# Kernel optimization log

Measured on AMD Instinct MI355X. Metric: run time of the kernel, lower is better.

## Reference

```python
import jax, jax.numpy as jnp
import numpy as np
from jax import lax

EPS = 1e-12
CLS_K = 100   # cls-token prefilter size (hardcoded in patch_reconstruction)
ALPHA = 0.6   # weighting of cls vs patch-EMD distance (hardcoded in source)


def _l2norm(x, axis):
    # torch.nn.functional.normalize: x / max(||x||_2, eps)
    n = jnp.sqrt(jnp.sum(x * x, axis=axis, keepdims=True))
    return x / jnp.maximum(n, EPS)


def setup_inputs() -> dict:
    key = jax.random.key(0)
    k1, k2, k3, k4 = jax.random.split(key, 4)
    B, N, C, G = 16, 128, 768, 2000
    return {
        "query_cls": jax.random.normal(k1, (B, C), dtype=jnp.float32),
        "query_patch": jax.random.normal(k2, (B, N, C), dtype=jnp.float32),
        "gallery_memory_cls": jax.random.normal(k3, (G, 1, C), dtype=jnp.float32),
        "gallery_memory_patch": jax.random.normal(k4, (G, N, C), dtype=jnp.float32),
        "top_k": 10,
    }


def reference(query_cls, query_patch, gallery_memory_cls, gallery_memory_patch, top_k):
    B, N, C = query_patch.shape
    g_cls = gallery_memory_cls[:, 0, :]          # [G, C] (torch.squeeze)
    g_cls_n = _l2norm(g_cls, axis=1)             # normalize(gallery_feat, dim=1)

    def per_sample(qc, qp):
        # --- stage 1: cls-token cosine prefilter (find_k_neighbors, metric='cls_token')
        qc_n = _l2norm(qc, axis=0)               # [C]
        dist_cls_all = g_cls_n @ qc_n            # [G] cosine sim
        _, cls_idx = lax.top_k(dist_cls_all, CLS_K)   # top-100 by cls sim

        # --- stage 2: combined cls + patch-EMD score over the 100 candidates
        sq = _l2norm(qp.T, axis=0)               # [C, N] per-patch unit norm
        gp = gallery_memory_patch[cls_idx]       # [K, N, C] gather
        gp_t = _l2norm(jnp.transpose(gp, (0, 2, 1)), axis=1)  # [K, C, N]
        # pairwise patch cosine sims: [K, Nq, Ng]
        sim = jnp.einsum('cn,kcm->knm', sq, gp_t)
        # bidirectional Chamfer similarity as the patch-EMD score
        dist_emd = 0.5 * (jnp.mean(jnp.max(sim, axis=2), axis=1)
                          + jnp.mean(jnp.max(sim, axis=1), axis=1))  # [K]
        dist_cls = dist_cls_all[cls_idx]         # [K]
        dist = ALPHA * dist_cls + (1.0 - ALPHA) * dist_emd
        _, emd_idx = lax.top_k(dist, top_k)      # top_k of 100 candidates
        nb = cls_idx[emd_idx]                    # [top_k] gallery indices

        # --- reconstruction: gather neighbor patches + mean neighbor cls
        patch = gallery_memory_patch[nb]         # [top_k, N, C]
        cls_m = jnp.mean(g_cls[nb], axis=0)      # [C]
        return patch.reshape(top_k * N, C), cls_m

    rec_patch, rec_cls = jax.vmap(per_sample)(query_cls, query_patch)
    return rec_patch, rec_cls[:, None, :]        # [B, top_k*N, C], [B, 1, C]
```

## Files before the change

kernel.cpp:

```cpp
#include <hip/hip_runtime.h>
#include <float.h>
#include <math.h>

#define B_ 16
#define N_ 128
#define C_ 768
#define G_ 2000
#define CK_ 100
#define ALPHA_ 0.6f
#define EPS_ 1e-12f

typedef __attribute__((ext_vector_type(8))) short bf16x8;
typedef __attribute__((ext_vector_type(16))) float f32x16;

__device__ inline float wave_sum_lane0(float s) {
  #pragma unroll
  for (int off = 32; off > 0; off >>= 1) s += __shfl_down(s, off);
  return s;
}
__device__ inline float wave_sum_all(float s) {
  #pragma unroll
  for (int off = 1; off < 64; off <<= 1) s += __shfl_xor(s, off);
  return s;
}

__device__ inline unsigned short bf16_rtn(float x) {
  unsigned u = __float_as_uint(x);
  u += 0x7fffu + ((u >> 16) & 1u);
  return (unsigned short)(u >> 16);
}
__device__ inline void split2(float x, unsigned short& h, unsigned short& l) {
  h = bf16_rtn(x);
  float r = x - __uint_as_float(((unsigned)h) << 16);
  l = bf16_rtn(r);
}
__device__ inline void csplit8(const float4& v0, const float4& v1,
                               uint4& h, uint4& l, float& sq) {
  float f[8] = {v0.x, v0.y, v0.z, v0.w, v1.x, v1.y, v1.z, v1.w};
  unsigned short hh[8], ll[8];
  #pragma unroll
  for (int i = 0; i < 8; ++i) {
    float x = f[i];
    sq = fmaf(x, x, sq);
    split2(x, hh[i], ll[i]);
  }
  h.x = (unsigned)hh[0] | ((unsigned)hh[1] << 16);
  h.y = (unsigned)hh[2] | ((unsigned)hh[3] << 16);
  h.z = (unsigned)hh[4] | ((unsigned)hh[5] << 16);
  h.w = (unsigned)hh[6] | ((unsigned)hh[7] << 16);
  l.x = (unsigned)ll[0] | ((unsigned)ll[1] << 16);
  l.y = (unsigned)ll[2] | ((unsigned)ll[3] << 16);
  l.z = (unsigned)ll[4] | ((unsigned)ll[5] << 16);
  l.w = (unsigned)ll[6] | ((unsigned)ll[7] << 16);
}

#define NCLSBLK_ (B_ * G_ / 4)
__global__ void prep_kernel(const float* __restrict__ gcls, const float* __restrict__ qcls,
                            const float* __restrict__ qp,
                            float* __restrict__ dall,
                            unsigned short* __restrict__ qhi, unsigned short* __restrict__ qlo) {
  int t = threadIdx.x;
  int lane = t & 63;
  if ((int)blockIdx.x < NCLSBLK_) {
    int id = ((int)blockIdx.x * 256 + t) >> 6;
    int b = id / G_, g = id - b * G_;
    const float4* gv = (const float4*)(gcls + (size_t)g * C_);
    const float4* qv = (const float4*)(qcls + (size_t)b * C_);
    float sgq = 0.f, sgg = 0.f, sqq = 0.f;
    #pragma unroll
    for (int i = 0; i < 3; ++i) {
      float4 x = gv[lane + 64 * i], y = qv[lane + 64 * i];
      sgq += x.x * y.x + x.y * y.y + x.z * y.z + x.w * y.w;
      sgg += x.x * x.x + x.y * x.y + x.z * x.z + x.w * x.w;
      sqq += y.x * y.x + y.y * y.y + y.z * y.z + y.w * y.w;
    }
    sgq = wave_sum_lane0(sgq);
    sgg = wave_sum_lane0(sgg);
    sqq = wave_sum_lane0(sqq);
    if (lane == 0) {
      float gi = 1.0f / fmaxf(sqrtf(sgg), EPS_);
      float qi = 1.0f / fmaxf(sqrtf(sqq), EPS_);
      dall[id] = sgq * gi * qi;
    }
  } else {
    int wid = (((int)blockIdx.x - NCLSBLK_) * 256 + t) >> 6;
    const float4* v = (const float4*)(qp + (size_t)wid * C_);
    float4 x0 = v[lane], x1 = v[lane + 64], x2 = v[lane + 128];
    float s = x0.x * x0.x + x0.y * x0.y + x0.z * x0.z + x0.w * x0.w
            + x1.x * x1.x + x1.y * x1.y + x1.z * x1.z + x1.w * x1.w
            + x2.x * x2.x + x2.y * x2.y + x2.z * x2.z + x2.w * x2.w;
    s = wave_sum_all(s);
    float inv = 1.0f / fmaxf(sqrtf(s), EPS_);
    float4 xs[3] = {x0, x1, x2};
    #pragma unroll
    for (int i = 0; i < 3; ++i) {
      float4 x = xs[i];
      x.x *= inv; x.y *= inv; x.z *= inv; x.w *= inv;
      ushort4 h, l;
      split2(x.x, h.x, l.x); split2(x.y, h.y, l.y);
      split2(x.z, h.z, l.z); split2(x.w, h.w, l.w);
      size_t off = (size_t)wid * C_ + (size_t)(lane + 64 * i) * 4;
      *(ushort4*)(qhi + off) = h;
      *(ushort4*)(qlo + off) = l;
    }
  }
}

__global__ void top100_kernel(const float* __restrict__ dall, int* __restrict__ cls_idx,
                              float* __restrict__ dsel) {
  __shared__ unsigned long long s[2048];
  int b = blockIdx.x, t = threadIdx.x;
  for (int i = t; i < 2048; i += 256) {
    unsigned long long y = 0xFFFFFFFFFFFFFFFFull;
    if (i < G_) {
      unsigned u = __float_as_uint(dall[b * G_ + i]);
      unsigned key = (u & 0x80000000u) ? ~u : (u | 0x80000000u);
      y = ~(((unsigned long long)key << 32) | (unsigned long long)(0xFFFFFFFFu - (unsigned)i));
    }
    s[i] = y;
  }
  __syncthreads();
  for (int k = 2; k <= 2048; k <<= 1) {
    for (int j = k >> 1; j > 0; j >>= 1) {
      for (int i = t; i < 2048; i += 256) {
        int l = i ^ j;
        if (l > i) {
          unsigned long long a = s[i], c = s[l];
          bool up = ((i & k) == 0);
          if ((a > c) == up) { s[i] = c; s[l] = a; }
        }
      }
      __syncthreads();
    }
  }
  for (int it = t; it < CK_; it += 256) {
    unsigned long long x = ~s[it];
    int idx = (int)(0xFFFFFFFFu - (unsigned)(x & 0xFFFFFFFFull));
    unsigned key = (unsigned)(x >> 32);
    unsigned u = (key & 0x80000000u) ? (key & 0x7FFFFFFFu) : ~key;
    cls_idx[b * CK_ + it] = idx;
    dsel[b * CK_ + it] = __uint_as_float(u);
  }
}

__global__ __launch_bounds__(256, 4) void emd_kernel(
    const unsigned short* __restrict__ qhi, const unsigned short* __restrict__ qlo,
    const float* __restrict__ gpat,
    const int* __restrict__ cls_idx, const float* __restrict__ dsel,
    float* __restrict__ dist) {
  __shared__ __align__(16) unsigned short sAhi[4096], sAlo[4096], sBhi[4096], sBlo[4096];
  float* red_row = (float*)&sAhi[0];
  float* red_col = (float*)&sAhi[512];
  float* bssp    = (float*)&sAhi[1024];
  float* binvp   = (float*)&sAhi[1536];

  int r = blockIdx.x;
  int xc = r & 7;
  int q = r >> 3;
  int b = 2 * xc + (q >= CK_ ? 1 : 0);
  int k = (q >= CK_) ? (q - CK_) : q;
  int blk = b * CK_ + k;
  int g = cls_idx[blk];

  const float* Bptr = gpat + (size_t)g * (N_ * C_);

  int t = threadIdx.x;
  int lane = t & 63, wv = t >> 6;
  int wr = wv >> 1, wc = wv & 1;
  int l31 = lane & 31, lhi = lane >> 5;

  int m_st = t >> 1, half = t & 1;
  const unsigned short* ahB = qhi + (size_t)(b * N_ + m_st) * C_ + half * 16;
  const unsigned short* alB = qlo + (size_t)(b * N_ + m_st) * C_ + half * 16;
  const float* bB = Bptr + (size_t)m_st * C_ + half * 16;
  int sw_st = (m_st >> 1) & 3;
  int e0 = m_st * 32 + (((2 * half + 0) ^ sw_st) << 3);
  int e1 = m_st * 32 + (((2 * half + 1) ^ sw_st) << 3);

  f32x16 acc00, acc01, acc10, acc11;
  #pragma unroll
  for (int e = 0; e < 16; ++e) { acc00[e] = 0.f; acc01[e] = 0.f; acc10[e] = 0.f; acc11[e] = 0.f; }

  int rA0 = 64 * wr + l31, rA1 = rA0 + 32;
  int rB0 = 64 * wc + l31, rB1 = rB0 + 32;
  int swF = (l31 >> 1) & 3;

  float4 cb0, cb1, cb2, cb3;
  cb0 = *(const float4*)(bB);      cb1 = *(const float4*)(bB + 4);
  cb2 = *(const float4*)(bB + 8);  cb3 = *(const float4*)(bB + 12);

  float bsq = 0.f;
  const int NT = C_ / 32;
  for (int kt = 0; kt < NT; ++kt) {
    __syncthreads();
    int o = kt * 32;
    uint4 va0 = *(const uint4*)(ahB + o);
    uint4 va1 = *(const uint4*)(ahB + o + 8);
    uint4 va2 = *(const uint4*)(alB + o);
    uint4 va3 = *(const uint4*)(alB + o + 8);
    uint4 h, l;
    csplit8(cb0, cb1, h, l, bsq);
    *(uint4*)&sBhi[e0] = h;  *(uint4*)&sBlo[e0] = l;
    csplit8(cb2, cb3, h, l, bsq);
    *(uint4*)&sBhi[e1] = h;  *(uint4*)&sBlo[e1] = l;
    *(uint4*)&sAhi[e0] = va0;  *(uint4*)&sAhi[e1] = va1;
    *(uint4*)&sAlo[e0] = va2;  *(uint4*)&sAlo[e1] = va3;
    if (kt + 1 < NT) {
      int o2 = o + 32;
      cb0 = *(const float4*)(bB + o2);       cb1 = *(const float4*)(bB + o2 + 4);
      cb2 = *(const float4*)(bB + o2 + 8);   cb3 = *(const float4*)(bB + o2 + 12);
    }
    __syncthreads();
    #pragma unroll
    for (int ks = 0; ks < 2; ++ks) {
      int so = (((ks * 2 + lhi) ^ swF) << 3);
      bf16x8 ah0 = *(const bf16x8*)&sAhi[rA0 * 32 + so];
      bf16x8 al0 = *(const bf16x8*)&sAlo[rA0 * 32 + so];
      bf16x8 ah1 = *(const bf16x8*)&sAhi[rA1 * 32 + so];
      bf16x8 al1 = *(const bf16x8*)&sAlo[rA1 * 32 + so];
      bf16x8 bh0 = *(const bf16x8*)&sBhi[rB0 * 32 + so];
      bf16x8 bl0 = *(const bf16x8*)&sBlo[rB0 * 32 + so];
      bf16x8 bh1 = *(const bf16x8*)&sBhi[rB1 * 32 + so];
      bf16x8 bl1 = *(const bf16x8*)&sBlo[rB1 * 32 + so];
      acc00 = __builtin_amdgcn_mfma_f32_32x32x16_bf16(ah0, bh0, acc00, 0, 0, 0);
      acc00 = __builtin_amdgcn_mfma_f32_32x32x16_bf16(ah0, bl0, acc00, 0, 0, 0);
      acc00 = __builtin_amdgcn_mfma_f32_32x32x16_bf16(al0, bh0, acc00, 0, 0, 0);
      acc01 = __builtin_amdgcn_mfma_f32_32x32x16_bf16(ah0, bh1, acc01, 0, 0, 0);
      acc01 = __builtin_amdgcn_mfma_f32_32x32x16_bf16(ah0, bl1, acc01, 0, 0, 0);
      acc01 = __builtin_amdgcn_mfma_f32_32x32x16_bf16(al0, bh1, acc01, 0, 0, 0);
      acc10 = __builtin_amdgcn_mfma_f32_32x32x16_bf16(ah1, bh0, acc10, 0, 0, 0);
      acc10 = __builtin_amdgcn_mfma_f32_32x32x16_bf16(ah1, bl0, acc10, 0, 0, 0);
      acc10 = __builtin_amdgcn_mfma_f32_32x32x16_bf16(al1, bh0, acc10, 0, 0, 0);
      acc11 = __builtin_amdgcn_mfma_f32_32x32x16_bf16(ah1, bh1, acc11, 0, 0, 0);
      acc11 = __builtin_amdgcn_mfma_f32_32x32x16_bf16(ah1, bl1, acc11, 0, 0, 0);
      acc11 = __builtin_amdgcn_mfma_f32_32x32x16_bf16(al1, bh1, acc11, 0, 0, 0);
    }
  }
  __syncthreads();

  bssp[t] = bsq;
  __syncthreads();
  if (t < 128) {
    float s = bssp[2 * t] + bssp[2 * t + 1];
    binvp[t] = 1.0f / fmaxf(sqrtf(s), EPS_);
  }
  __syncthreads();
  float bi0 = binvp[64 * wc + l31];
  float bi1 = binvp[64 * wc + 32 + l31];

  {
    float rm[16];
    #pragma unroll
    for (int e = 0; e < 16; ++e) rm[e] = fmaxf(acc00[e] * bi0, acc01[e] * bi1);
    #pragma unroll
    for (int msk = 1; msk <= 16; msk <<= 1)
      #pragma unroll
      for (int e = 0; e < 16; ++e) rm[e] = fmaxf(rm[e], __shfl_xor(rm[e], msk));
    if (l31 == 0) {
      #pragma unroll
      for (int e = 0; e < 16; ++e)
        red_row[(64 * wr + (e & 3) + 8 * (e >> 2) + 4 * lhi) * 2 + wc] = rm[e];
    }
  }
  {
    float rm[16];
    #pragma unroll
    for (int e = 0; e < 16; ++e) rm[e] = fmaxf(acc10[e] * bi0, acc11[e] * bi1);
    #pragma unroll
    for (int msk = 1; msk <= 16; msk <<= 1)
      #pragma unroll
      for (int e = 0; e < 16; ++e) rm[e] = fmaxf(rm[e], __shfl_xor(rm[e], msk));
    if (l31 == 0) {
      #pragma unroll
      for (int e = 0; e < 16; ++e)
        red_row[(64 * wr + 32 + (e & 3) + 8 * (e >> 2) + 4 * lhi) * 2 + wc] = rm[e];
    }
  }
  {
    float cm0 = -FLT_MAX, cm1 = -FLT_MAX;
    #pragma unroll
    for (int e = 0; e < 16; ++e) {
      cm0 = fmaxf(cm0, fmaxf(acc00[e], acc10[e]));
      cm1 = fmaxf(cm1, fmaxf(acc01[e], acc11[e]));
    }
    cm0 = fmaxf(cm0, __shfl_xor(cm0, 32)) * bi0;
    cm1 = fmaxf(cm1, __shfl_xor(cm1, 32)) * bi1;
    if (lane < 32) {
      red_col[(64 * wc + lane) * 2 + wr] = cm0;
      red_col[(64 * wc + 32 + lane) * 2 + wr] = cm1;
    }
  }
  __syncthreads();
  if (t < 128)
    bssp[t] = fmaxf(red_row[2 * t], red_row[2 * t + 1]) +
              fmaxf(red_col[2 * t], red_col[2 * t + 1]);
  __syncthreads();
  if (t < 64) {
    float v = bssp[t] + bssp[t + 64];
    #pragma unroll
    for (int off = 32; off > 0; off >>= 1) v += __shfl_down(v, off);
    if (t == 0) {
      float emd = 0.5f * v * (1.0f / 128.0f);
      dist[blk] = ALPHA_ * dsel[blk] + (1.0f - ALPHA_) * emd;
    }
  }
}

__global__ void sel10_kernel(const float* __restrict__ dist, const int* __restrict__ cls_idx,
                             const float* __restrict__ gcls, float* __restrict__ out_cls,
                             int* __restrict__ nb, int TK) {
  int b = blockIdx.x, t = threadIdx.x;
  __shared__ float v[128];
  __shared__ int snb[64];
  if (t < 128) v[t] = (t < CK_) ? dist[b * CK_ + t] : -FLT_MAX;
  __syncthreads();
  for (int j = 0; j < TK; ++j) {
    if (t < 64) {
      float v0 = v[t], v1 = v[t + 64];
      float bv; int bi;
      if (v0 >= v1) { bv = v0; bi = t; } else { bv = v1; bi = t + 64; }
      #pragma unroll
      for (int off = 1; off < 64; off <<= 1) {
        float ov = __shfl_xor(bv, off);
        int   oi = __shfl_xor(bi, off);
        if (ov > bv || (ov == bv && oi < bi)) { bv = ov; bi = oi; }
      }
      if (t == 0) {
        int gg = cls_idx[b * CK_ + bi];
        snb[j] = gg;
        nb[b * TK + j] = gg;
        v[bi] = -FLT_MAX;
      }
    }
    __syncthreads();
  }
  float invk = 1.0f / (float)TK;
  for (int c = t; c < C_; c += 256) {
    float s = 0.f;
    for (int j = 0; j < TK; ++j) s += gcls[(size_t)snb[j] * C_ + c];
    out_cls[(size_t)b * C_ + c] = s * invk;
  }
}

__global__ void gather_kernel(const float* __restrict__ gpat, const int* __restrict__ nb,
                              float* __restrict__ out, int TK) {
  int i = blockIdx.x * blockDim.x + threadIdx.x;
  int per_vec = N_ * C_ / 4;
  int per_b = TK * per_vec;
  int total = B_ * per_b;
  if (i >= total) return;
  int b = i / per_b;
  int r = i - b * per_b;
  int j = r / per_vec;
  int off = r - j * per_vec;
  int g = nb[b * TK + j];
  ((float4*)out)[i] = ((const float4*)gpat)[(size_t)g * per_vec + off];
}

extern "C" void kernel_launch(void* const* d_in, const int* in_sizes, int n_in,
                              void* d_out, int out_size, void* d_ws, size_t ws_size,
                              hipStream_t stream) {
  (void)in_sizes; (void)n_in; (void)ws_size;
  const float* qcls = (const float*)d_in[0];
  const float* qpat = (const float*)d_in[1];
  const float* gcls = (const float*)d_in[2];
  const float* gpat = (const float*)d_in[3];
  int TK = (out_size / B_ - C_) / (N_ * C_);

  unsigned short* qhi = (unsigned short*)d_ws;
  unsigned short* qlo = qhi + (size_t)B_ * N_ * C_;
  float* dall  = (float*)(qlo + (size_t)B_ * N_ * C_);
  float* dsel  = dall + B_ * G_;
  float* dist  = dsel + B_ * CK_;
  int* cls_idx = (int*)(dist + B_ * CK_);
  int* nb      = cls_idx + B_ * CK_;

  hipLaunchKernelGGL(prep_kernel, dim3(NCLSBLK_ + B_ * N_ / 4), dim3(256), 0, stream,
                     gcls, qcls, qpat, dall, qhi, qlo);
  hipLaunchKernelGGL(top100_kernel, dim3(B_), dim3(256), 0, stream, dall, cls_idx, dsel);
  hipLaunchKernelGGL(emd_kernel, dim3(B_ * CK_), dim3(256), 0, stream,
                     qhi, qlo, gpat, cls_idx, dsel, dist);
  float* out_cls = (float*)d_out + (size_t)B_ * TK * N_ * C_;
  hipLaunchKernelGGL(sel10_kernel, dim3(B_), dim3(256), 0, stream,
                     dist, cls_idx, gcls, out_cls, nb, TK);
  int total4 = B_ * TK * (N_ * C_ / 4);
  hipLaunchKernelGGL(gather_kernel, dim3((total4 + 255) / 256), dim3(256), 0, stream,
                     gpat, nb, (float*)d_out, TK);
}
```

Baseline: 320.5 us.

## Use 512-thread blocks in EMD kernel with 8 waves each computing 64x32 tiles

Moves the EMD similarity kernel from 4 waves per block, each holding a 64x64 output tile, to 8 waves per block, each holding a 64x32 tile. The staging loads are spread over twice as many threads, and the query tile loads are now prefetched one step ahead along with the gallery loads. The per-row norm reduction and the row and column max reductions are rewritten for the new wave grid. The aim is more waves in flight to hide memory latency and fewer accumulator registers per thread, at the cost of more LDS reads per MFMA and a 512-thread launch bound that may limit how many blocks fit per CU.

```diff
diff --git a/kernel.cpp b/kernel.cpp
--- a/kernel.cpp
+++ b/kernel.cpp
@@ -143,16 +143,16 @@
   }
 }
 
-__global__ __launch_bounds__(256, 4) void emd_kernel(
+__global__ __launch_bounds__(512, 4) void emd_kernel(
     const unsigned short* __restrict__ qhi, const unsigned short* __restrict__ qlo,
     const float* __restrict__ gpat,
     const int* __restrict__ cls_idx, const float* __restrict__ dsel,
     float* __restrict__ dist) {
   __shared__ __align__(16) unsigned short sAhi[4096], sAlo[4096], sBhi[4096], sBlo[4096];
   float* red_row = (float*)&sAhi[0];
-  float* red_col = (float*)&sAhi[512];
-  float* bssp    = (float*)&sAhi[1024];
-  float* binvp   = (float*)&sAhi[1536];
+  float* red_col = (float*)&sAhi[1024];
+  float* bssp    = (float*)&sAhi[1536];
+  float* binvp   = (float*)&sAhi[1792];
 
   int r = blockIdx.x;
   int xc = r & 7;
@@ -166,49 +166,47 @@
 
   int t = threadIdx.x;
   int lane = t & 63, wv = t >> 6;
-  int wr = wv >> 1, wc = wv & 1;
+  int wr = wv >> 2, wc = wv & 3;
   int l31 = lane & 31, lhi = lane >> 5;
 
-  int m_st = t >> 1, half = t & 1;
-  const unsigned short* ahB = qhi + (size_t)(b * N_ + m_st) * C_ + half * 16;
-  const unsigned short* alB = qlo + (size_t)(b * N_ + m_st) * C_ + half * 16;
-  const float* bB = Bptr + (size_t)m_st * C_ + half * 16;
+  int m_st = t >> 2, quar = t & 3;
+  const unsigned short* ahB = qhi + (size_t)(b * N_ + m_st) * C_ + quar * 8;
+  const unsigned short* alB = qlo + (size_t)(b * N_ + m_st) * C_ + quar * 8;
+  const float* bB = Bptr + (size_t)m_st * C_ + quar * 8;
   int sw_st = (m_st >> 1) & 3;
-  int e0 = m_st * 32 + (((2 * half + 0) ^ sw_st) << 3);
-  int e1 = m_st * 32 + (((2 * half + 1) ^ sw_st) << 3);
-
-  f32x16 acc00, acc01, acc10, acc11;
+  int e0 = m_st * 32 + ((quar ^ sw_st) << 3);
+
+  f32x16 acc0, acc1;
   #pragma unroll
-  for (int e = 0; e < 16; ++e) { acc00[e] = 0.f; acc01[e] = 0.f; acc10[e] = 0.f; acc11[e] = 0.f; }
+  for (int e = 0; e < 16; ++e) { acc0[e] = 0.f; acc1[e] = 0.f; }
 
   int rA0 = 64 * wr + l31, rA1 = rA0 + 32;
-  int rB0 = 64 * wc + l31, rB1 = rB0 + 32;
+  int rB0 = 32 * wc + l31;
   int swF = (l31 >> 1) & 3;
 
-  float4 cb0, cb1, cb2, cb3;
-  cb0 = *(const float4*)(bB);      cb1 = *(const float4*)(bB + 4);
-  cb2 = *(const float4*)(bB + 8);  cb3 = *(const float4*)(bB + 12);
+  uint4 cah, cal;
+  float4 cb0, cb1;
+  cah = *(const uint4*)(ahB);
+  cal = *(const uint4*)(alB);
+  cb0 = *(const float4*)(bB);
+  cb1 = *(const float4*)(bB + 4);
 
   float bsq = 0.f;
   const int NT = C_ / 32;
   for (int kt = 0; kt < NT; ++kt) {
     __syncthreads();
-    int o = kt * 32;
-    uint4 va0 = *(const uint4*)(ahB + o);
-    uint4 va1 = *(const uint4*)(ahB + o + 8);
-    uint4 va2 = *(const uint4*)(alB + o);
-    uint4 va3 = *(const uint4*)(alB + o + 8);
+    *(uint4*)&sAhi[e0] = cah;
+    *(uint4*)&sAlo[e0] = cal;
     uint4 h, l;
     csplit8(cb0, cb1, h, l, bsq);
-    *(uint4*)&sBhi[e0] = h;  *(uint4*)&sBlo[e0] = l;
-    csplit8(cb2, cb3, h, l, bsq);
-    *(uint4*)&sBhi[e1] = h;  *(uint4*)&sBlo[e1] = l;
-    *(uint4*)&sAhi[e0] = va0;  *(uint4*)&sAhi[e1] = va1;
-    *(uint4*)&sAlo[e0] = va2;  *(uint4*)&sAlo[e1] = va3;
+    *(uint4*)&sBhi[e0] = h;
+    *(uint4*)&sBlo[e0] = l;
     if (kt + 1 < NT) {
-      int o2 = o + 32;
-      cb0 = *(const float4*)(bB + o2);       cb1 = *(const float4*)(bB + o2 + 4);
-      cb2 = *(const float4*)(bB + o2 + 8);   cb3 = *(const float4*)(bB + o2 + 12);
+      int o = (kt + 1) * 32;
+      cah = *(const uint4*)(ahB + o);
+      cal = *(const uint4*)(alB + o);
+      cb0 = *(const float4*)(bB + o);
+      cb1 = *(const float4*)(bB + o + 4);
     }
     __syncthreads();
     #pragma unroll
@@ -220,38 +218,26 @@
       bf16x8 al1 = *(const bf16x8*)&sAlo[rA1 * 32 + so];
       bf16x8 bh0 = *(const bf16x8*)&sBhi[rB0 * 32 + so];
       bf16x8 bl0 = *(const bf16x8*)&sBlo[rB0 * 32 + so];
-      bf16x8 bh1 = *(const bf16x8*)&sBhi[rB1 * 32 + so];
-      bf16x8 bl1 = *(const bf16x8*)&sBlo[rB1 * 32 + so];
-      acc00 = __builtin_amdgcn_mfma_f32_32x32x16_bf16(ah0, bh0, acc00, 0, 0, 0);
-      acc00 = __builtin_amdgcn_mfma_f32_32x32x16_bf16(ah0, bl0, acc00, 0, 0, 0);
-      acc00 = __builtin_amdgcn_mfma_f32_32x32x16_bf16(al0, bh0, acc00, 0, 0, 0);
-      acc01 = __builtin_amdgcn_mfma_f32_32x32x16_bf16(ah0, bh1, acc01, 0, 0, 0);
-      acc01 = __builtin_amdgcn_mfma_f32_32x32x16_bf16(ah0, bl1, acc01, 0, 0, 0);
-      acc01 = __builtin_amdgcn_mfma_f32_32x32x16_bf16(al0, bh1, acc01, 0, 0, 0);
-      acc10 = __builtin_amdgcn_mfma_f32_32x32x16_bf16(ah1, bh0, acc10, 0, 0, 0);
-      acc10 = __builtin_amdgcn_mfma_f32_32x32x16_bf16(ah1, bl0, acc10, 0, 0, 0);
-      acc10 = __builtin_amdgcn_mfma_f32_32x32x16_bf16(al1, bh0, acc10, 0, 0, 0);
-      acc11 = __builtin_amdgcn_mfma_f32_32x32x16_bf16(ah1, bh1, acc11, 0, 0, 0);
-      acc11 = __builtin_amdgcn_mfma_f32_32x32x16_bf16(ah1, bl1, acc11, 0, 0, 0);
-      acc11 = __builtin_amdgcn_mfma_f32_32x32x16_bf16(al1, bh1, acc11, 0, 0, 0);
-    }
-  }
-  __syncthreads();
-
-  bssp[t] = bsq;
-  __syncthreads();
-  if (t < 128) {
-    float s = bssp[2 * t] + bssp[2 * t + 1];
-    binvp[t] = 1.0f / fmaxf(sqrtf(s), EPS_);
-  }
-  __syncthreads();
-  float bi0 = binvp[64 * wc + l31];
-  float bi1 = binvp[64 * wc + 32 + l31];
+      acc0 = __builtin_amdgcn_mfma_f32_32x32x16_bf16(ah0, bh0, acc0, 0, 0, 0);
+      acc0 = __builtin_amdgcn_mfma_f32_32x32x16_bf16(ah0, bl0, acc0, 0, 0, 0);
+      acc0 = __builtin_amdgcn_mfma_f32_32x32x16_bf16(al0, bh0, acc0, 0, 0, 0);
+      acc1 = __builtin_amdgcn_mfma_f32_32x32x16_bf16(ah1, bh0, acc1, 0, 0, 0);
+      acc1 = __builtin_amdgcn_mfma_f32_32x32x16_bf16(ah1, bl0, acc1, 0, 0, 0);
+      acc1 = __builtin_amdgcn_mfma_f32_32x32x16_bf16(al1, bh0, acc1, 0, 0, 0);
+    }
+  }
+  __syncthreads();
+
+  bsq += __shfl_xor(bsq, 1);
+  bsq += __shfl_xor(bsq, 2);
+  if ((t & 3) == 0) binvp[m_st] = 1.0f / fmaxf(sqrtf(bsq), EPS_);
+  __syncthreads();
+  float bi0 = binvp[rB0];
 
   {
     float rm[16];
     #pragma unroll
-    for (int e = 0; e < 16; ++e) rm[e] = fmaxf(acc00[e] * bi0, acc01[e] * bi1);
+    for (int e = 0; e < 16; ++e) rm[e] = acc0[e] * bi0;
     #pragma unroll
     for (int msk = 1; msk <= 16; msk <<= 1)
       #pragma unroll
@@ -259,13 +245,13 @@
     if (l31 == 0) {
       #pragma unroll
       for (int e = 0; e < 16; ++e)
-        red_row[(64 * wr + (e & 3) + 8 * (e >> 2) + 4 * lhi) * 2 + wc] = rm[e];
+        red_row[(64 * wr + (e & 3) + 8 * (e >> 2) + 4 * lhi) * 4 + wc] = rm[e];
     }
   }
   {
     float rm[16];
     #pragma unroll
-    for (int e = 0; e < 16; ++e) rm[e] = fmaxf(acc10[e] * bi0, acc11[e] * bi1);
+    for (int e = 0; e < 16; ++e) rm[e] = acc1[e] * bi0;
     #pragma unroll
     for (int msk = 1; msk <= 16; msk <<= 1)
       #pragma unroll
@@ -273,27 +259,23 @@
     if (l31 == 0) {
       #pragma unroll
       for (int e = 0; e < 16; ++e)
-        red_row[(64 * wr + 32 + (e & 3) + 8 * (e >> 2) + 4 * lhi) * 2 + wc] = rm[e];
+        red_row[(64 * wr + 32 + (e & 3) + 8 * (e >> 2) + 4 * lhi) * 4 + wc] = rm[e];
     }
   }
   {
-    float cm0 = -FLT_MAX, cm1 = -FLT_MAX;
-    #pragma unroll
-    for (int e = 0; e < 16; ++e) {
-      cm0 = fmaxf(cm0, fmaxf(acc00[e], acc10[e]));
-      cm1 = fmaxf(cm1, fmaxf(acc01[e], acc11[e]));
-    }
-    cm0 = fmaxf(cm0, __shfl_xor(cm0, 32)) * bi0;
-    cm1 = fmaxf(cm1, __shfl_xor(cm1, 32)) * bi1;
-    if (lane < 32) {
-      red_col[(64 * wc + lane) * 2 + wr] = cm0;
-      red_col[(64 * wc + 32 + lane) * 2 + wr] = cm1;
-    }
-  }
-  __syncthreads();
-  if (t < 128)
-    bssp[t] = fmaxf(red_row[2 * t], red_row[2 * t + 1]) +
-              fmaxf(red_col[2 * t], red_col[2 * t + 1]);
+    float cm = -FLT_MAX;
+    #pragma unroll
+    for (int e = 0; e < 16; ++e) cm = fmaxf(cm, fmaxf(acc0[e], acc1[e]));
+    cm = fmaxf(cm, __shfl_xor(cm, 32)) * bi0;
+    if (lane < 32) red_col[(32 * wc + lane) * 2 + wr] = cm;
+  }
+  __syncthreads();
+  if (t < 128) {
+    float r4 = fmaxf(fmaxf(red_row[4 * t], red_row[4 * t + 1]),
+                     fmaxf(red_row[4 * t + 2], red_row[4 * t + 3]));
+    float c2 = fmaxf(red_col[2 * t], red_col[2 * t + 1]);
+    bssp[t] = r4 + c2;
+  }
   __syncthreads();
   if (t < 64) {
     float v = bssp[t] + bssp[t + 64];
@@ -378,7 +360,7 @@
   hipLaunchKernelGGL(prep_kernel, dim3(NCLSBLK_ + B_ * N_ / 4), dim3(256), 0, stream,
                      gcls, qcls, qpat, dall, qhi, qlo);
   hipLaunchKernelGGL(top100_kernel, dim3(B_), dim3(256), 0, stream, dall, cls_idx, dsel);
-  hipLaunchKernelGGL(emd_kernel, dim3(B_ * CK_), dim3(256), 0, stream,
+  hipLaunchKernelGGL(emd_kernel, dim3(B_ * CK_), dim3(512), 0, stream,
                      qhi, qlo, gpat, cls_idx, dsel, dist);
   float* out_cls = (float*)d_out + (size_t)B_ * TK * N_ * C_;
   hipLaunchKernelGGL(sel10_kernel, dim3(B_), dim3(256), 0, stream,
```

Result: faster. 312.4 us (-2.5%).

## Double-buffer LDS tiles in EMD kernel and use truncation for bf16 split

Applied to the files above, without the earlier changes.

The EMD GEMM main loop now uses two LDS buffers, so staging the next K-tile overlaps with the MFMA work on the current one, with one barrier per tile instead of two. Global loads for B are prefetched two tiles ahead in alternating register sets. The hi/lo bf16 split now truncates the high part instead of rounding to nearest, which cuts integer ALU work but changes precision behaviour slightly (the lo residual is also truncated). LDS use doubles to 64KB and launch bounds drop to 2 blocks per CU, which may reduce occupancy.

```diff
diff --git a/kernel.cpp b/kernel.cpp
--- a/kernel.cpp
+++ b/kernel.cpp
@@ -34,24 +34,24 @@
   float r = x - __uint_as_float(((unsigned)h) << 16);
   l = bf16_rtn(r);
 }
-__device__ inline void csplit8(const float4& v0, const float4& v1,
+__device__ inline void tsplit8(const float4& v0, const float4& v1,
                                uint4& h, uint4& l, float& sq) {
   float f[8] = {v0.x, v0.y, v0.z, v0.w, v1.x, v1.y, v1.z, v1.w};
-  unsigned short hh[8], ll[8];
+  unsigned hu[4], lu[4];
   #pragma unroll
-  for (int i = 0; i < 8; ++i) {
-    float x = f[i];
-    sq = fmaf(x, x, sq);
-    split2(x, hh[i], ll[i]);
-  }
-  h.x = (unsigned)hh[0] | ((unsigned)hh[1] << 16);
-  h.y = (unsigned)hh[2] | ((unsigned)hh[3] << 16);
-  h.z = (unsigned)hh[4] | ((unsigned)hh[5] << 16);
-  h.w = (unsigned)hh[6] | ((unsigned)hh[7] << 16);
-  l.x = (unsigned)ll[0] | ((unsigned)ll[1] << 16);
-  l.y = (unsigned)ll[2] | ((unsigned)ll[3] << 16);
-  l.z = (unsigned)ll[4] | ((unsigned)ll[5] << 16);
-  l.w = (unsigned)ll[6] | ((unsigned)ll[7] << 16);
+  for (int p = 0; p < 4; ++p) {
+    float x0 = f[2 * p], x1 = f[2 * p + 1];
+    sq = fmaf(x0, x0, sq);
+    sq = fmaf(x1, x1, sq);
+    unsigned u0 = __float_as_uint(x0), u1 = __float_as_uint(x1);
+    float r0 = x0 - __uint_as_float(u0 & 0xFFFF0000u);
+    float r1 = x1 - __uint_as_float(u1 & 0xFFFF0000u);
+    unsigned v0b = __float_as_uint(r0), v1b = __float_as_uint(r1);
+    hu[p] = (u0 >> 16) | (u1 & 0xFFFF0000u);
+    lu[p] = (v0b >> 16) | (v1b & 0xFFFF0000u);
+  }
+  h = make_uint4(hu[0], hu[1], hu[2], hu[3]);
+  l = make_uint4(lu[0], lu[1], lu[2], lu[3]);
 }
 
 #define NCLSBLK_ (B_ * G_ / 4)
@@ -143,16 +143,17 @@
   }
 }
 
-__global__ __launch_bounds__(256, 4) void emd_kernel(
+__global__ __launch_bounds__(256, 2) void emd_kernel(
     const unsigned short* __restrict__ qhi, const unsigned short* __restrict__ qlo,
     const float* __restrict__ gpat,
     const int* __restrict__ cls_idx, const float* __restrict__ dsel,
     float* __restrict__ dist) {
-  __shared__ __align__(16) unsigned short sAhi[4096], sAlo[4096], sBhi[4096], sBlo[4096];
-  float* red_row = (float*)&sAhi[0];
-  float* red_col = (float*)&sAhi[512];
-  float* bssp    = (float*)&sAhi[1024];
-  float* binvp   = (float*)&sAhi[1536];
+  __shared__ __align__(16) unsigned short sAhi[2][4096], sAlo[2][4096];
+  __shared__ __align__(16) unsigned short sBhi[2][4096], sBlo[2][4096];
+  float* red_row = (float*)&sAhi[0][0];
+  float* red_col = (float*)&sAhi[0][512];
+  float* bssf    = (float*)&sAhi[0][1024];
+  float* binvf   = (float*)&sAhi[0][1536];
 
   int r = blockIdx.x;
   int xc = r & 7;
@@ -185,68 +186,96 @@
   int rB0 = 64 * wc + l31, rB1 = rB0 + 32;
   int swF = (l31 >> 1) & 3;
 
-  float4 cb0, cb1, cb2, cb3;
-  cb0 = *(const float4*)(bB);      cb1 = *(const float4*)(bB + 4);
-  cb2 = *(const float4*)(bB + 8);  cb3 = *(const float4*)(bB + 12);
+  const int NT = C_ / 32;
 
   float bsq = 0.f;
-  const int NT = C_ / 32;
-  for (int kt = 0; kt < NT; ++kt) {
+
+  uint4 cah0, cah1, cal0, cal1;
+  float4 bx0, bx1, bx2, bx3, by0, by1, by2, by3;
+
+#define LOAD_A(T) { int oA = (T) * 32;                                        \
+    cah0 = *(const uint4*)(ahB + oA);  cah1 = *(const uint4*)(ahB + oA + 8);  \
+    cal0 = *(const uint4*)(alB + oA);  cal1 = *(const uint4*)(alB + oA + 8); }
+#define LOAD_BX(T) { int oB = (T) * 32;                                       \
+    bx0 = *(const float4*)(bB + oB);      bx1 = *(const float4*)(bB + oB + 4);\
+    bx2 = *(const float4*)(bB + oB + 8);  bx3 = *(const float4*)(bB + oB + 12); }
+#define LOAD_BY(T) { int oB = (T) * 32;                                       \
+    by0 = *(const float4*)(bB + oB);      by1 = *(const float4*)(bB + oB + 4);\
+    by2 = *(const float4*)(bB + oB + 8);  by3 = *(const float4*)(bB + oB + 12); }
+
+#define STAGE(P, Bq0, Bq1, Bq2, Bq3) {                                        \
+    uint4 h, l;                                                               \
+    tsplit8(Bq0, Bq1, h, l, bsq);                                             \
+    *(uint4*)&sBhi[P][e0] = h;  *(uint4*)&sBlo[P][e0] = l;                    \
+    tsplit8(Bq2, Bq3, h, l, bsq);                                             \
+    *(uint4*)&sBhi[P][e1] = h;  *(uint4*)&sBlo[P][e1] = l;                    \
+    *(uint4*)&sAhi[P][e0] = cah0;  *(uint4*)&sAhi[P][e1] = cah1;              \
+    *(uint4*)&sAlo[P][e0] = cal0;  *(uint4*)&sAlo[P][e1] = cal1;              \
+  }
+
+#define MFMA_PHASE(P)                                                         \
+  _Pragma("unroll")                                                           \
+  for (int ks = 0; ks < 2; ++ks) {                                            \
+    int so = (((ks * 2 + lhi) ^ swF) << 3);                                   \
+    bf16x8 ah0 = *(const bf16x8*)&sAhi[P][rA0 * 32 + so];                     \
+    bf16x8 al0 = *(const bf16x8*)&sAlo[P][rA0 * 32 + so];                     \
+    bf16x8 ah1 = *(const bf16x8*)&sAhi[P][rA1 * 32 + so];                     \
+    bf16x8 al1 = *(const bf16x8*)&sAlo[P][rA1 * 32 + so];                     \
+    bf16x8 bh0 = *(const bf16x8*)&sBhi[P][rB0 * 32 + so];                     \
+    bf16x8 bl0 = *(const bf16x8*)&sBlo[P][rB0 * 32 + so];                     \
+    bf16x8 bh1 = *(const bf16x8*)&sBhi[P][rB1 * 32 + so];                     \
+    bf16x8 bl1 = *(const bf16x8*)&sBlo[P][rB1 * 32 + so];                     \
+    acc00 = __builtin_amdgcn_mfma_f32_32x32x16_bf16(ah0, bh0, acc00, 0, 0, 0);\
+    acc00 = __builtin_amdgcn_mfma_f32_32x32x16_bf16(ah0, bl0, acc00, 0, 0, 0);\
+    acc00 = __builtin_amdgcn_mfma_f32_32x32x16_bf16(al0, bh0, acc00, 0, 0, 0);\
+    acc01 = __builtin_amdgcn_mfma_f32_32x32x16_bf16(ah0, bh1, acc01, 0, 0, 0);\
+    acc01 = __builtin_amdgcn_mfma_f32_32x32x16_bf16(ah0, bl1, acc01, 0, 0, 0);\
+    acc01 = __builtin_amdgcn_mfma_f32_32x32x16_bf16(al0, bh1, acc01, 0, 0, 0);\
+    acc10 = __builtin_amdgcn_mfma_f32_32x32x16_bf16(ah1, bh0, acc10, 0, 0, 0);\
+    acc10 = __builtin_amdgcn_mfma_f32_32x32x16_bf16(ah1, bl0, acc10, 0, 0, 0);\
+    acc10 = __builtin_amdgcn_mfma_f32_32x32x16_bf16(al1, bh0, acc10, 0, 0, 0);\
+    acc11 = __builtin_amdgcn_mfma_f32_32x32x16_bf16(ah1, bh1, acc11, 0, 0, 0);\
+    acc11 = __builtin_amdgcn_mfma_f32_32x32x16_bf16(ah1, bl1, acc11, 0, 0, 0);\
+    acc11 = __builtin_amdgcn_mfma_f32_32x32x16_bf16(al1, bh1, acc11, 0, 0, 0);\
+  }
+
+  LOAD_A(0);
+  LOAD_BX(0);
+  LOAD_BY(1);
+  STAGE(0, bx0, bx1, bx2, bx3);
+  LOAD_A(1);
+  LOAD_BX(2);
+  __syncthreads();
+
+  for (int kt = 0; kt < NT; kt += 2) {
+    if (kt + 1 < NT) STAGE(1, by0, by1, by2, by3);
+    if (kt + 2 < NT) LOAD_A(kt + 2);
+    if (kt + 3 < NT) LOAD_BY(kt + 3);
+    MFMA_PHASE(0);
     __syncthreads();
-    int o = kt * 32;
-    uint4 va0 = *(const uint4*)(ahB + o);
-    uint4 va1 = *(const uint4*)(ahB + o + 8);
-    uint4 va2 = *(const uint4*)(alB + o);
-    uint4 va3 = *(const uint4*)(alB + o + 8);
-    uint4 h, l;
-    csplit8(cb0, cb1, h, l, bsq);
-    *(uint4*)&sBhi[e0] = h;  *(uint4*)&sBlo[e0] = l;
-    csplit8(cb2, cb3, h, l, bsq);
-    *(uint4*)&sBhi[e1] = h;  *(uint4*)&sBlo[e1] = l;
-    *(uint4*)&sAhi[e0] = va0;  *(uint4*)&sAhi[e1] = va1;
-    *(uint4*)&sAlo[e0] = va2;  *(uint4*)&sAlo[e1] = va3;
     if (kt + 1 < NT) {
-      int o2 = o + 32;
-      cb0 = *(const float4*)(bB + o2);       cb1 = *(const float4*)(bB + o2 + 4);
-      cb2 = *(const float4*)(bB + o2 + 8);   cb3 = *(const float4*)(bB + o2 + 12);
+      if (kt + 2 < NT) STAGE(0, bx0, bx1, bx2, bx3);
+      if (kt + 3 < NT) LOAD_A(kt + 3);
+      if (kt + 4 < NT) LOAD_BX(kt + 4);
+      MFMA_PHASE(1);
     }
     __syncthreads();
-    #pragma unroll
-    for (int ks = 0; ks < 2; ++ks) {
-      int so = (((ks * 2 + lhi) ^ swF) << 3);
-      bf16x8 ah0 = *(const bf16x8*)&sAhi[rA0 * 32 + so];
-      bf16x8 al0 = *(const bf16x8*)&sAlo[rA0 * 32 + so];
-      bf16x8 ah1 = *(const bf16x8*)&sAhi[rA1 * 32 + so];
-      bf16x8 al1 = *(const bf16x8*)&sAlo[rA1 * 32 + so];
-      bf16x8 bh0 = *(const bf16x8*)&sBhi[rB0 * 32 + so];
-      bf16x8 bl0 = *(const bf16x8*)&sBlo[rB0 * 32 + so];
-      bf16x8 bh1 = *(const bf16x8*)&sBhi[rB1 * 32 + so];
-      bf16x8 bl1 = *(const bf16x8*)&sBlo[rB1 * 32 + so];
-      acc00 = __builtin_amdgcn_mfma_f32_32x32x16_bf16(ah0, bh0, acc00, 0, 0, 0);
-      acc00 = __builtin_amdgcn_mfma_f32_32x32x16_bf16(ah0, bl0, acc00, 0, 0, 0);
-      acc00 = __builtin_amdgcn_mfma_f32_32x32x16_bf16(al0, bh0, acc00, 0, 0, 0);
-      acc01 = __builtin_amdgcn_mfma_f32_32x32x16_bf16(ah0, bh1, acc01, 0, 0, 0);
-      acc01 = __builtin_amdgcn_mfma_f32_32x32x16_bf16(ah0, bl1, acc01, 0, 0, 0);
-      acc01 = __builtin_amdgcn_mfma_f32_32x32x16_bf16(al0, bh1, acc01, 0, 0, 0);
-      acc10 = __builtin_amdgcn_mfma_f32_32x32x16_bf16(ah1, bh0, acc10, 0, 0, 0);
-      acc10 = __builtin_amdgcn_mfma_f32_32x32x16_bf16(ah1, bl0, acc10, 0, 0, 0);
-      acc10 = __builtin_amdgcn_mfma_f32_32x32x16_bf16(al1, bh0, acc10, 0, 0, 0);
-      acc11 = __builtin_amdgcn_mfma_f32_32x32x16_bf16(ah1, bh1, acc11, 0, 0, 0);
-      acc11 = __builtin_amdgcn_mfma_f32_32x32x16_bf16(ah1, bl1, acc11, 0, 0, 0);
-      acc11 = __builtin_amdgcn_mfma_f32_32x32x16_bf16(al1, bh1, acc11, 0, 0, 0);
-    }
-  }
-  __syncthreads();
-
-  bssp[t] = bsq;
+  }
+#undef LOAD_A
+#undef LOAD_BX
+#undef LOAD_BY
+#undef STAGE
+#undef MFMA_PHASE
+
+  bssf[t] = bsq;
   __syncthreads();
   if (t < 128) {
-    float s = bssp[2 * t] + bssp[2 * t + 1];
-    binvp[t] = 1.0f / fmaxf(sqrtf(s), EPS_);
-  }
-  __syncthreads();
-  float bi0 = binvp[64 * wc + l31];
-  float bi1 = binvp[64 * wc + 32 + l31];
+    float s = bssf[2 * t] + bssf[2 * t + 1];
+    binvf[t] = 1.0f / fmaxf(sqrtf(s), EPS_);
+  }
+  __syncthreads();
+  float bi0 = binvf[64 * wc + l31];
+  float bi1 = binvf[64 * wc + 32 + l31];
 
   {
     float rm[16];
@@ -292,11 +321,11 @@
   }
   __syncthreads();
   if (t < 128)
-    bssp[t] = fmaxf(red_row[2 * t], red_row[2 * t + 1]) +
+    bssf[t] = fmaxf(red_row[2 * t], red_row[2 * t + 1]) +
               fmaxf(red_col[2 * t], red_col[2 * t + 1]);
   __syncthreads();
   if (t < 64) {
-    float v = bssp[t] + bssp[t + 64];
+    float v = bssf[t] + bssf[t + 64];
     #pragma unroll
     for (int off = 32; off > 0; off >>= 1) v += __shfl_down(v, off);
     if (t == 0) {
```

Result: no change. 315.0 us (-1.7%).
